# Optimization experiments

Hardware: AMD Instinct MI355X
Metric: run time of the kernel (lower is better)

The kernel has to match this reference:

```python
import jax, jax.numpy as jnp
import numpy as np

B, S, D_IN, D_OUT, H = 2, 2048, 1024, 1024, 16
HD = D_OUT // H

def setup_inputs() -> dict:
    key = jax.random.key(0)
    ks = jax.random.split(key, 6)
    sc_in = 1.0 / np.sqrt(D_IN)
    sc_out = 1.0 / np.sqrt(D_OUT)
    return {
        "x": jax.random.normal(ks[0], (B, S, D_IN), dtype=jnp.float32),
        "Wq": jax.random.uniform(ks[1], (D_IN, D_OUT), jnp.float32, -sc_in, sc_in),
        "Wk": jax.random.uniform(ks[2], (D_IN, D_OUT), jnp.float32, -sc_in, sc_in),
        "Wv": jax.random.uniform(ks[3], (D_IN, D_OUT), jnp.float32, -sc_in, sc_in),
        "Wo": jax.random.uniform(ks[4], (D_OUT, D_OUT), jnp.float32, -sc_out, sc_out),
        "bo": jax.random.uniform(ks[5], (D_OUT,), jnp.float32, -sc_out, sc_out),
    }

def reference(x, Wq, Wk, Wv, Wo, bo):
    b, s, _ = x.shape
    # QKV projections (no bias), split heads -> [b, h, s, hd]
    q = (x @ Wq).reshape(b, s, H, HD).transpose(0, 2, 1, 3)
    k = (x @ Wk).reshape(b, s, H, HD).transpose(0, 2, 1, 3)
    v = (x @ Wv).reshape(b, s, H, HD).transpose(0, 2, 1, 3)
    scores = jnp.einsum('bhqd,bhkd->bhqk', q, k)
    causal = jnp.triu(jnp.ones((s, s), dtype=bool), k=1)
    scores = jnp.where(causal, -jnp.inf, scores)
    w = jax.nn.softmax(scores / np.sqrt(HD), axis=-1)  # dropout p=0.0 -> identity
    ctx = jnp.einsum('bhqk,bhkd->bhqd', w, v)
    ctx = ctx.transpose(0, 2, 1, 3).reshape(b, s, D_OUT)
    return ctx @ Wo + bo
```

## Files before the change

kernel.cpp:

```cpp
#include <hip/hip_runtime.h>
#include <stdint.h>

typedef unsigned short u16;
typedef __attribute__((ext_vector_type(8))) short short8;
typedef __attribute__((ext_vector_type(4))) float floatx4;
typedef __attribute__((ext_vector_type(4))) u16 ushort4v;

typedef __attribute__((address_space(1))) const uint32_t gu32;
typedef __attribute__((address_space(3))) uint32_t lu32;

#define MFMA(a, b, c) __builtin_amdgcn_mfma_f32_16x16x32_bf16((a), (b), (c), 0, 0, 0)

__device__ __forceinline__ u16 f2bf(float f) {
    union { float f; uint32_t u; } x; x.f = f;
    uint32_t u = x.u;
    u += 0x7fffu + ((u >> 16) & 1u);
    return (u16)(u >> 16);
}

__device__ __forceinline__ uint32_t cvtpk_bf16(float lo, float hi) {
    uint32_t r;
    asm("v_cvt_pk_bf16_f32 %0, %1, %2" : "=v"(r) : "v"(lo), "v"(hi));
    return r;
}

__device__ __forceinline__ float fexp2(float x) {
#if defined(__has_builtin)
#if __has_builtin(__builtin_amdgcn_exp2f)
    return __builtin_amdgcn_exp2f(x);
#else
    return exp2f(x);
#endif
#else
    return exp2f(x);
#endif
}

__device__ __forceinline__ void async16(u16* lds, const u16* g) {
    __builtin_amdgcn_global_load_lds((gu32*)g, (lu32*)lds, 16, 0, 0);
}

#define KV8(buf, row, byteInRow) \
    (*(short8*)((char*)(buf) + (((row) << 7) + ((byteInRow) ^ (((row) & 7) << 4)))))

#define Q_SCALE_LOG2E 0.18033688011112042f

__global__ __launch_bounds__(256) void prep_kernel(
    const float* __restrict__ x,
    const float* __restrict__ W0, const float* __restrict__ W1,
    const float* __restrict__ W2, const float* __restrict__ W3,
    u16* __restrict__ WT, u16* __restrict__ Xbf)
{
    const int z = blockIdx.z;
    const int tx = threadIdx.x, ty = threadIdx.y;
    if (z == 4) {
        const int bid = blockIdx.y * 32 + blockIdx.x;
        const int t = ty * 32 + tx;
        const size_t base = ((size_t)bid * 256 + t) * 16;
        const float* xf = x + base;
        short8 v0, v1;
#pragma unroll
        for (int j = 0; j < 8; j++) v0[j] = (short)f2bf(xf[j]);
#pragma unroll
        for (int j = 0; j < 8; j++) v1[j] = (short)f2bf(xf[8 + j]);
        *(short8*)&Xbf[base] = v0;
        *(short8*)&Xbf[base + 8] = v1;
        return;
    }
    __shared__ u16 tile[32][33];
    const float* W = (z == 0) ? W0 : (z == 1) ? W1 : (z == 2) ? W2 : W3;
    u16* dst = WT + (size_t)z * 1024 * 1024;
    const int n0 = blockIdx.x * 32, k0 = blockIdx.y * 32;
#pragma unroll
    for (int i = 0; i < 4; i++)
        tile[ty + i * 8][tx] = f2bf(W[(size_t)(k0 + ty + i * 8) * 1024 + n0 + tx]);
    __syncthreads();
#pragma unroll
    for (int i = 0; i < 4; i++)
        dst[(size_t)(n0 + ty + i * 8) * 1024 + k0 + tx] = tile[tx][ty + i * 8];
}

#define GSTAGE64(buf, gptr, kk) do { \
    _Pragma("unroll") \
    for (int i_ = 0; i_ < 4; i_++) \
        async16((buf) + wave * 512 + i_ * 2048, (gptr) + (kk) + (size_t)i_ * 32 * 1024); \
} while (0)

#define GFRAG64(buf, base, ks, fr) \
    (*(const short8*)&(buf)[((base) + (fr) * 16 + lrow) * 64 + ((((ks) * 4 + lquad) ^ (lrow & 7)) * 8)])

#define GCOMPUTE64() do { \
    _Pragma("unroll") \
    for (int ks = 0; ks < 2; ks++) { \
        short8 af[4], bfv[4]; \
        _Pragma("unroll") \
        for (int mt = 0; mt < 4; mt++) af[mt] = GFRAG64(As, wr, ks, mt); \
        _Pragma("unroll") \
        for (int nt = 0; nt < 4; nt++) bfv[nt] = GFRAG64(Bs, wc, ks, nt); \
        _Pragma("unroll") \
        for (int mt = 0; mt < 4; mt++) \
            _Pragma("unroll") \
            for (int nt = 0; nt < 4; nt++) \
                acc[mt][nt] = MFMA(af[mt], bfv[nt], acc[mt][nt]); \
    } \
} while (0)

#define GEMM_K_LOOP64() do { \
    for (int kk = 0; kk < 1024; kk += 64) { \
        __syncthreads(); \
        GSTAGE64(As, gA, kk); \
        GSTAGE64(Bs, gB, kk); \
        __syncthreads(); \
        GCOMPUTE64(); \
    } \
} while (0)

__global__ __launch_bounds__(256) void gemm_qkv_kernel(
    const u16* __restrict__ X, const u16* __restrict__ WT,
    u16* __restrict__ Q, u16* __restrict__ Kout, u16* __restrict__ VT)
{
    __shared__ __align__(16) u16 As[128 * 64];
    __shared__ __align__(16) u16 Bs[128 * 64];
    const int bid = blockIdx.x;
    const int xcd = bid & 7;
    const int idx = bid >> 3;
    const int mat = idx >> 5;
    const int rr  = (idx >> 3) & 3;
    const int nn  = idx & 7;
    const int m0 = (xcd * 4 + rr) * 128;
    const int n0 = nn * 128;
    const u16* BW = WT + (size_t)mat * 1024 * 1024;
    const int tid = threadIdx.x;
    const int wave = tid >> 6, lane = tid & 63;
    const int lrow = lane & 15, lquad = lane >> 4;
    const int wr = (wave >> 1) * 64, wc = (wave & 1) * 64;

    const int stg_r = tid >> 3;
    const int stg_c = ((tid & 7) ^ ((tid >> 3) & 7)) * 8;
    const u16* gA = &X[(size_t)(m0 + stg_r) * 1024 + stg_c];
    const u16* gB = &BW[(size_t)(n0 + stg_r) * 1024 + stg_c];

    floatx4 acc[4][4];
#pragma unroll
    for (int mt = 0; mt < 4; mt++)
#pragma unroll
        for (int nt = 0; nt < 4; nt++) acc[mt][nt] = (floatx4){0.f, 0.f, 0.f, 0.f};

    GEMM_K_LOOP64();

    const float qs = (mat == 0) ? Q_SCALE_LOG2E : 1.0f;
#pragma unroll
    for (int mt = 0; mt < 4; mt++) {
        const int gm = m0 + wr + mt * 16 + lquad * 4;
        const int b_ = gm >> 11;
        const int s  = gm & 2047;
#pragma unroll
        for (int nt = 0; nt < 4; nt++) {
            const int gn = n0 + wc + nt * 16 + lrow;
            const int h = gn >> 6, hd = gn & 63;
            const int bh = b_ * 16 + h;
            if (mat == 2) {
                ushort4v v;
#pragma unroll
                for (int i = 0; i < 4; i++) v[i] = f2bf(acc[mt][nt][i]);
                *(ushort4v*)&VT[((size_t)bh * 64 + hd) * 2048 + s] = v;
            } else {
                u16* dst = (mat == 0) ? Q : Kout;
#pragma unroll
                for (int i = 0; i < 4; i++)
                    dst[((size_t)bh * 2048 + s + i) * 64 + hd] = f2bf(acc[mt][nt][i] * qs);
            }
        }
    }
}

__global__ __launch_bounds__(256, 3) void attn_kernel(
    const u16* __restrict__ Q, const u16* __restrict__ Kk,
    const u16* __restrict__ VT, u16* __restrict__ ctx)
{
    __shared__ __align__(16) u16 Ks[2][64 * 64];
    __shared__ __align__(16) u16 Vs[2][64 * 64];
    __shared__ __align__(16) u16 P[4][16][72];
    const int tid = threadIdx.x, wave = tid >> 6, lane = tid & 63;
    const int lrow = lane & 15, lquad = lane >> 4;
    const float NEGINF = -__builtin_inff();

    const int bh = blockIdx.x & 31;
    const int g = blockIdx.x >> 5;
    const int qb = (g < 16) ? (31 - g) : (g - 16);
    const int ntiles = qb + 1;
    const int q0 = qb * 64 + wave * 16;

    const u16* Qb = Q  + (size_t)bh * 2048 * 64;
    const u16* Kb = Kk + (size_t)bh * 2048 * 64;
    const u16* Vb = VT + (size_t)bh * 64 * 2048;

    const short8 qf0 = *(const short8*)&Qb[(size_t)(q0 + lrow) * 64 + lquad * 8];
    const short8 qf1 = *(const short8*)&Qb[(size_t)(q0 + lrow) * 64 + 32 + lquad * 8];

    const int myq = q0 + lrow;
    float m_s = NEGINF, l_s = 0.f;
    floatx4 o[4];
#pragma unroll
    for (int i = 0; i < 4; i++) o[i] = (floatx4){0.f, 0.f, 0.f, 0.f};

    const int r0 = tid >> 3, r1 = r0 + 32;
    const int ce = (tid & 7) * 8;
    const int cb = (tid & 7) * 16;

    short8 kreg0 = *(const short8*)&Kb[(size_t)r0 * 64 + ce];
    short8 kreg1 = *(const short8*)&Kb[(size_t)r1 * 64 + ce];
    short8 vreg0 = *(const short8*)&Vb[(size_t)r0 * 2048 + ce];
    short8 vreg1 = *(const short8*)&Vb[(size_t)r1 * 2048 + ce];

    for (int kt = 0; kt < ntiles; kt++) {
        u16* Kc = Ks[kt & 1];
        u16* Vc = Vs[kt & 1];
        KV8(Kc, r0, cb) = kreg0;
        KV8(Kc, r1, cb) = kreg1;
        KV8(Vc, r0, cb) = vreg0;
        KV8(Vc, r1, cb) = vreg1;
        if (kt + 1 < ntiles) {
            kreg0 = *(const short8*)&Kb[(size_t)((kt + 1) * 64 + r0) * 64 + ce];
            kreg1 = *(const short8*)&Kb[(size_t)((kt + 1) * 64 + r1) * 64 + ce];
            vreg0 = *(const short8*)&Vb[(size_t)r0 * 2048 + (kt + 1) * 64 + ce];
            vreg1 = *(const short8*)&Vb[(size_t)r1 * 2048 + (kt + 1) * 64 + ce];
        }
        __syncthreads();

        floatx4 s[4];
#pragma unroll
        for (int nt = 0; nt < 4; nt++) {
            const short8 kf0 = KV8(Kc, nt * 16 + lrow, lquad * 16);
            const short8 kf1 = KV8(Kc, nt * 16 + lrow, 64 + lquad * 16);
            floatx4 a = (floatx4){0.f, 0.f, 0.f, 0.f};
            a = MFMA(kf0, qf0, a);
            a = MFMA(kf1, qf1, a);
            s[nt] = a;
        }

        if (kt == ntiles - 1) {
#pragma unroll
            for (int nt = 0; nt < 4; nt++)
#pragma unroll
                for (int i = 0; i < 4; i++)
                    if (kt * 64 + nt * 16 + lquad * 4 + i > myq) s[nt][i] = NEGINF;
        }

        float mx = NEGINF;
#pragma unroll
        for (int nt = 0; nt < 4; nt++)
            mx = fmaxf(mx, fmaxf(fmaxf(s[nt][0], s[nt][1]),
                                 fmaxf(s[nt][2], s[nt][3])));
        mx = fmaxf(mx, __shfl_xor(mx, 16));
        mx = fmaxf(mx, __shfl_xor(mx, 32));

        if (!__all(mx <= m_s + 8.0f)) {
            const float mnew = fmaxf(m_s, mx);
            const float alpha = fexp2(m_s - mnew);
            m_s = mnew;
            l_s *= alpha;
#pragma unroll
            for (int ht = 0; ht < 4; ht++)
#pragma unroll
                for (int i = 0; i < 4; i++) o[ht][i] *= alpha;
        }

        float sum = 0.f;
#pragma unroll
        for (int nt = 0; nt < 4; nt++)
#pragma unroll
            for (int i = 0; i < 4; i++) {
                const float pv = fexp2(s[nt][i] - m_s);
                s[nt][i] = pv;
                sum += pv;
            }
        sum += __shfl_xor(sum, 16);
        sum += __shfl_xor(sum, 32);
        l_s += sum;

#pragma unroll
        for (int nt = 0; nt < 4; nt++) {
            uint2 pk;
            pk.x = cvtpk_bf16(s[nt][0], s[nt][1]);
            pk.y = cvtpk_bf16(s[nt][2], s[nt][3]);
            *(uint2*)&P[wave][lrow][nt * 16 + lquad * 4] = pk;
        }
#pragma unroll
        for (int st = 0; st < 2; st++) {
            const short8 pf = *(const short8*)&P[wave][lrow][st * 32 + lquad * 8];
#pragma unroll
            for (int ht = 0; ht < 4; ht++) {
                const short8 vf = KV8(Vc, ht * 16 + lrow, st * 64 + lquad * 16);
                o[ht] = MFMA(vf, pf, o[ht]);
            }
        }
    }

    const int b_ = bh >> 4, h_ = bh & 15;
    const float inv_l = 1.0f / l_s;
#pragma unroll
    for (int ht = 0; ht < 4; ht++) {
        uint2 pk;
        pk.x = cvtpk_bf16(o[ht][0] * inv_l, o[ht][1] * inv_l);
        pk.y = cvtpk_bf16(o[ht][2] * inv_l, o[ht][3] * inv_l);
        *(uint2*)&ctx[((size_t)(b_ * 2048 + q0 + lrow)) * 1024 + h_ * 64 + ht * 16 + lquad * 4] = pk;
    }
}

__global__ __launch_bounds__(256) void gemm_out_kernel(
    const u16* __restrict__ X, const u16* __restrict__ WT,
    const float* __restrict__ bias, float* __restrict__ out)
{
    __shared__ __align__(16) u16 As[128 * 64];
    __shared__ __align__(16) u16 Bs[128 * 64];
    const int bid = blockIdx.x;
    const int xcd = bid & 7;
    const int idx = bid >> 3;
    const int rr  = idx >> 3;
    const int nn  = idx & 7;
    const int m0 = (xcd * 4 + rr) * 128;
    const int n0 = nn * 128;
    const int tid = threadIdx.x;
    const int wave = tid >> 6, lane = tid & 63;
    const int lrow = lane & 15, lquad = lane >> 4;
    const int wr = (wave >> 1) * 64, wc = (wave & 1) * 64;

    const int stg_r = tid >> 3;
    const int stg_c = ((tid & 7) ^ ((tid >> 3) & 7)) * 8;
    const u16* gA = &X[(size_t)(m0 + stg_r) * 1024 + stg_c];
    const u16* gB = &WT[(size_t)(n0 + stg_r) * 1024 + stg_c];

    floatx4 acc[4][4];
#pragma unroll
    for (int mt = 0; mt < 4; mt++)
#pragma unroll
        for (int nt = 0; nt < 4; nt++) acc[mt][nt] = (floatx4){0.f, 0.f, 0.f, 0.f};

    GEMM_K_LOOP64();

#pragma unroll
    for (int mt = 0; mt < 4; mt++) {
        const int gm = m0 + wr + mt * 16 + lquad * 4;
#pragma unroll
        for (int nt = 0; nt < 4; nt++) {
            const int gn = n0 + wc + nt * 16 + lrow;
            const float bv = bias[gn];
#pragma unroll
            for (int i = 0; i < 4; i++)
                out[(size_t)(gm + i) * 1024 + gn] = acc[mt][nt][i] + bv;
        }
    }
}

extern "C" void kernel_launch(void* const* d_in, const int* in_sizes, int n_in,
                              void* d_out, int out_size, void* d_ws, size_t ws_size,
                              hipStream_t stream) {
    u16* ws = (u16*)d_ws + 64;

    const size_t MB1 = 1024 * 1024;
    u16* WT   = ws;
    u16* Qw   = ws + 4 * MB1;
    u16* Kw   = ws + 8 * MB1;
    u16* VTw  = ws + 12 * MB1;
    u16* ctxw = ws + 16 * MB1;
    u16* Xbf  = ws + 20 * MB1;

    prep_kernel<<<dim3(32, 32, 5), dim3(32, 8), 0, stream>>>(
        (const float*)d_in[0], (const float*)d_in[1], (const float*)d_in[2],
        (const float*)d_in[3], (const float*)d_in[4], WT, Xbf);
    gemm_qkv_kernel<<<768, 256, 0, stream>>>(Xbf, WT, Qw, Kw, VTw);
    attn_kernel<<<1024, 256, 0, stream>>>(Qw, Kw, VTw, ctxw);
    gemm_out_kernel<<<256, 256, 0, stream>>>(ctxw, WT + 3 * MB1, (const float*)d_in[5], (float*)d_out);
}
```

Measured before the change: 177.5 us.

## Process 128 query rows per attention block, two 16-row subtiles per wave

Each attention workgroup now covers 128 queries instead of 64, and each wave handles two 16-row query subtiles against the same shared K/V tiles. The grid is halved to 512 blocks. This doubles the reuse of every K/V tile loaded into shared memory, cutting global loads and barriers per unit of work. In exchange, register pressure rises with the duplicated accumulators and softmax state, and there are fewer blocks to balance the causal workload across CUs.

```diff
diff --git a/kernel.cpp b/kernel.cpp
--- a/kernel.cpp
+++ b/kernel.cpp
@@ -174,6 +174,70 @@
     }
 }
 
+#define SOFTPV(qfa, qfb, myq, m_s, l_s, o) do { \
+    floatx4 s[4]; \
+    _Pragma("unroll") \
+    for (int nt = 0; nt < 4; nt++) { \
+        const short8 kf0 = KV8(Kc, nt * 16 + lrow, lquad * 16); \
+        const short8 kf1 = KV8(Kc, nt * 16 + lrow, 64 + lquad * 16); \
+        floatx4 a = (floatx4){0.f, 0.f, 0.f, 0.f}; \
+        a = MFMA(kf0, (qfa), a); \
+        a = MFMA(kf1, (qfb), a); \
+        s[nt] = a; \
+    } \
+    if (kt >= ntiles - 2) {    \
+        _Pragma("unroll") \
+        for (int nt = 0; nt < 4; nt++) \
+            _Pragma("unroll") \
+            for (int i = 0; i < 4; i++) \
+                if (kt * 64 + nt * 16 + lquad * 4 + i > (myq)) s[nt][i] = NEGINF; \
+    } \
+    float mx = NEGINF; \
+    _Pragma("unroll") \
+    for (int nt = 0; nt < 4; nt++) \
+        mx = fmaxf(mx, fmaxf(fmaxf(s[nt][0], s[nt][1]), fmaxf(s[nt][2], s[nt][3]))); \
+    mx = fmaxf(mx, __shfl_xor(mx, 16)); \
+    mx = fmaxf(mx, __shfl_xor(mx, 32)); \
+    if (!__all(mx <= (m_s) + 8.0f)) {    \
+        const float mnew = fmaxf((m_s), mx); \
+        const float alpha = fexp2((m_s) - mnew); \
+        (m_s) = mnew; \
+        (l_s) *= alpha; \
+        _Pragma("unroll") \
+        for (int ht = 0; ht < 4; ht++) \
+            _Pragma("unroll") \
+            for (int i = 0; i < 4; i++) (o)[ht][i] *= alpha; \
+    } \
+    float sum = 0.f; \
+    _Pragma("unroll") \
+    for (int nt = 0; nt < 4; nt++) \
+        _Pragma("unroll") \
+        for (int i = 0; i < 4; i++) { \
+            const float pv = fexp2(s[nt][i] - (m_s)); \
+            s[nt][i] = pv; \
+            sum += pv; \
+        } \
+    sum += __shfl_xor(sum, 16); \
+    sum += __shfl_xor(sum, 32); \
+    (l_s) += sum; \
+    _Pragma("unroll") \
+    for (int nt = 0; nt < 4; nt++) { \
+        uint2 pk; \
+        pk.x = cvtpk_bf16(s[nt][0], s[nt][1]); \
+        pk.y = cvtpk_bf16(s[nt][2], s[nt][3]); \
+        *(uint2*)&P[wave][lrow][nt * 16 + lquad * 4] = pk; \
+    } \
+    _Pragma("unroll") \
+    for (int st = 0; st < 2; st++) { \
+        const short8 pf = *(const short8*)&P[wave][lrow][st * 32 + lquad * 8]; \
+        _Pragma("unroll") \
+        for (int ht = 0; ht < 4; ht++) { \
+            const short8 vf = KV8(Vc, ht * 16 + lrow, st * 64 + lquad * 16); \
+            (o)[ht] = MFMA(vf, pf, (o)[ht]); \
+        } \
+    } \
+} while (0)
+
 __global__ __launch_bounds__(256, 3) void attn_kernel(
     const u16* __restrict__ Q, const u16* __restrict__ Kk,
     const u16* __restrict__ VT, u16* __restrict__ ctx)
@@ -187,22 +251,27 @@
 
     const int bh = blockIdx.x & 31;
     const int g = blockIdx.x >> 5;
-    const int qb = (g < 16) ? (31 - g) : (g - 16);
-    const int ntiles = qb + 1;
-    const int q0 = qb * 64 + wave * 16;
+    const int qb = (g < 8) ? (15 - g) : (g - 8);
+    const int ntiles = 2 * qb + 2;
+    const int q0 = qb * 128 + wave * 32;
 
     const u16* Qb = Q  + (size_t)bh * 2048 * 64;
     const u16* Kb = Kk + (size_t)bh * 2048 * 64;
     const u16* Vb = VT + (size_t)bh * 64 * 2048;
 
-    const short8 qf0 = *(const short8*)&Qb[(size_t)(q0 + lrow) * 64 + lquad * 8];
-    const short8 qf1 = *(const short8*)&Qb[(size_t)(q0 + lrow) * 64 + 32 + lquad * 8];
-
-    const int myq = q0 + lrow;
-    float m_s = NEGINF, l_s = 0.f;
-    floatx4 o[4];
-#pragma unroll
-    for (int i = 0; i < 4; i++) o[i] = (floatx4){0.f, 0.f, 0.f, 0.f};
+    const short8 qf00 = *(const short8*)&Qb[(size_t)(q0 + lrow) * 64 + lquad * 8];
+    const short8 qf01 = *(const short8*)&Qb[(size_t)(q0 + lrow) * 64 + 32 + lquad * 8];
+    const short8 qf10 = *(const short8*)&Qb[(size_t)(q0 + 16 + lrow) * 64 + lquad * 8];
+    const short8 qf11 = *(const short8*)&Qb[(size_t)(q0 + 16 + lrow) * 64 + 32 + lquad * 8];
+
+    const int myq0 = q0 + lrow, myq1 = q0 + 16 + lrow;
+    float m0 = NEGINF, l0 = 0.f, m1 = NEGINF, l1 = 0.f;
+    floatx4 o0[4], o1[4];
+#pragma unroll
+    for (int i = 0; i < 4; i++) {
+        o0[i] = (floatx4){0.f, 0.f, 0.f, 0.f};
+        o1[i] = (floatx4){0.f, 0.f, 0.f, 0.f};
+    }
 
     const int r0 = tid >> 3, r1 = r0 + 32;
     const int ce = (tid & 7) * 8;
@@ -228,83 +297,22 @@
         }
         __syncthreads();
 
-        floatx4 s[4];
-#pragma unroll
-        for (int nt = 0; nt < 4; nt++) {
-            const short8 kf0 = KV8(Kc, nt * 16 + lrow, lquad * 16);
-            const short8 kf1 = KV8(Kc, nt * 16 + lrow, 64 + lquad * 16);
-            floatx4 a = (floatx4){0.f, 0.f, 0.f, 0.f};
-            a = MFMA(kf0, qf0, a);
-            a = MFMA(kf1, qf1, a);
-            s[nt] = a;
-        }
-
-        if (kt == ntiles - 1) {
-#pragma unroll
-            for (int nt = 0; nt < 4; nt++)
-#pragma unroll
-                for (int i = 0; i < 4; i++)
-                    if (kt * 64 + nt * 16 + lquad * 4 + i > myq) s[nt][i] = NEGINF;
-        }
-
-        float mx = NEGINF;
-#pragma unroll
-        for (int nt = 0; nt < 4; nt++)
-            mx = fmaxf(mx, fmaxf(fmaxf(s[nt][0], s[nt][1]),
-                                 fmaxf(s[nt][2], s[nt][3])));
-        mx = fmaxf(mx, __shfl_xor(mx, 16));
-        mx = fmaxf(mx, __shfl_xor(mx, 32));
-
-        if (!__all(mx <= m_s + 8.0f)) {
-            const float mnew = fmaxf(m_s, mx);
-            const float alpha = fexp2(m_s - mnew);
-            m_s = mnew;
-            l_s *= alpha;
-#pragma unroll
-            for (int ht = 0; ht < 4; ht++)
-#pragma unroll
-                for (int i = 0; i < 4; i++) o[ht][i] *= alpha;
-        }
-
-        float sum = 0.f;
-#pragma unroll
-        for (int nt = 0; nt < 4; nt++)
-#pragma unroll
-            for (int i = 0; i < 4; i++) {
-                const float pv = fexp2(s[nt][i] - m_s);
-                s[nt][i] = pv;
-                sum += pv;
-            }
-        sum += __shfl_xor(sum, 16);
-        sum += __shfl_xor(sum, 32);
-        l_s += sum;
-
-#pragma unroll
-        for (int nt = 0; nt < 4; nt++) {
-            uint2 pk;
-            pk.x = cvtpk_bf16(s[nt][0], s[nt][1]);
-            pk.y = cvtpk_bf16(s[nt][2], s[nt][3]);
-            *(uint2*)&P[wave][lrow][nt * 16 + lquad * 4] = pk;
-        }
-#pragma unroll
-        for (int st = 0; st < 2; st++) {
-            const short8 pf = *(const short8*)&P[wave][lrow][st * 32 + lquad * 8];
-#pragma unroll
-            for (int ht = 0; ht < 4; ht++) {
-                const short8 vf = KV8(Vc, ht * 16 + lrow, st * 64 + lquad * 16);
-                o[ht] = MFMA(vf, pf, o[ht]);
-            }
-        }
+        SOFTPV(qf00, qf01, myq0, m0, l0, o0);
+        SOFTPV(qf10, qf11, myq1, m1, l1, o1);
     }
 
     const int b_ = bh >> 4, h_ = bh & 15;
-    const float inv_l = 1.0f / l_s;
+    const float inv0 = 1.0f / l0;
+    const float inv1 = 1.0f / l1;
 #pragma unroll
     for (int ht = 0; ht < 4; ht++) {
         uint2 pk;
-        pk.x = cvtpk_bf16(o[ht][0] * inv_l, o[ht][1] * inv_l);
-        pk.y = cvtpk_bf16(o[ht][2] * inv_l, o[ht][3] * inv_l);
+        pk.x = cvtpk_bf16(o0[ht][0] * inv0, o0[ht][1] * inv0);
+        pk.y = cvtpk_bf16(o0[ht][2] * inv0, o0[ht][3] * inv0);
         *(uint2*)&ctx[((size_t)(b_ * 2048 + q0 + lrow)) * 1024 + h_ * 64 + ht * 16 + lquad * 4] = pk;
+        pk.x = cvtpk_bf16(o1[ht][0] * inv1, o1[ht][1] * inv1);
+        pk.y = cvtpk_bf16(o1[ht][2] * inv1, o1[ht][3] * inv1);
+        *(uint2*)&ctx[((size_t)(b_ * 2048 + q0 + 16 + lrow)) * 1024 + h_ * 64 + ht * 16 + lquad * 4] = pk;
     }
 }
 
@@ -370,6 +378,6 @@
         (const float*)d_in[0], (const float*)d_in[1], (const float*)d_in[2],
         (const float*)d_in[3], (const float*)d_in[4], WT, Xbf);
     gemm_qkv_kernel<<<768, 256, 0, stream>>>(Xbf, WT, Qw, Kw, VTw);
-    attn_kernel<<<1024, 256, 0, stream>>>(Qw, Kw, VTw, ctxw);
+    attn_kernel<<<512, 256, 0, stream>>>(Qw, Kw, VTw, ctxw);
     gemm_out_kernel<<<256, 256, 0, stream>>>(ctxw, WT + 3 * MB1, (const float*)d_in[5], (float*)d_out);
 }
```

Measured after the change: 189.3 us. +6.7%, slower.
